# Optimization experiments

Hardware: AMD Instinct MI355X
Metric: run time of the kernel (lower is better)

## Reference

```python
import jax, jax.numpy as jnp
import numpy as np

# module hyperparameters (match init_kwargs)
PATCH = 4          # patch_size
STRIDE = 2         # patch_stride
CH = 64            # embedding_dim (latent channels)
N_ATOMS = 512      # num_embeddings
SPARSITY = 5       # sparsity_level
COMMIT = 0.25      # commitment_cost
EPS = 1e-10        # epsilon
PATCH_DIM = CH * PATCH * PATCH


def _hann(n):
    # torch.hann_window(periodic=False)
    return 0.5 * (1.0 - jnp.cos(2.0 * jnp.pi * jnp.arange(n, dtype=jnp.float32) / (n - 1)))


def setup_inputs() -> dict:
    key = jax.random.key(0)
    k1, k2 = jax.random.split(key)
    x = jax.random.normal(k1, (8, CH, 128, 128), dtype=jnp.float32)
    D = jax.random.normal(k2, (PATCH_DIM, N_ATOMS), dtype=jnp.float32) * 0.02
    # normalize_dictionary_(): L2-normalize atoms (columns)
    D = D / jnp.maximum(jnp.linalg.norm(D, axis=0, keepdims=True), EPS)
    return {"x": x, "dictionary": D}


def reference(x, dictionary):
    B, C, H, W = x.shape
    Ho = (H - PATCH) // STRIDE + 1
    Wo = (W - PATCH) // STRIDE + 1
    N = B * Ho * Wo

    # ---- unfold (im2col) : [B,C,Ho,Wo,P,P] ----
    row = (jnp.arange(Ho) * STRIDE)[:, None] + jnp.arange(PATCH)  # [Ho,P]
    col = (jnp.arange(Wo) * STRIDE)[:, None] + jnp.arange(PATCH)  # [Wo,P]
    ridx = row[:, None, :, None]   # [Ho,1,P,1]
    cidx = col[None, :, None, :]   # [1,Wo,1,P]
    patches = x[:, :, ridx, cidx]  # [B,C,Ho,Wo,P,P]
    # columns ordered (C, ph, pw) like torch F.unfold
    X = patches.transpose(0, 2, 3, 1, 4, 5).reshape(N, PATCH_DIM)  # [N, patch_dim]

    # ---- batch_topk_with_support sparse coding ----
    corr = X @ dictionary                 # [N, K]  (D^T X)^T
    gram = dictionary.T @ dictionary      # [K, K]
    support = jax.lax.top_k(jnp.abs(corr), SPARSITY)[1]           # [N, k]
    rhs = jnp.take_along_axis(corr, support, axis=1)              # [N, k]
    gram_sup = gram[support[:, :, None], support[:, None, :]]     # [N, k, k]
    gram_sup = gram_sup + EPS * jnp.eye(SPARSITY, dtype=x.dtype)
    values = jnp.linalg.solve(gram_sup, rhs[..., None])[..., 0]   # [N, k]

    # ---- reconstruct patch signals: X_hat = D[:,support] @ values ----
    codes = jnp.zeros((N, N_ATOMS), dtype=x.dtype).at[
        jnp.arange(N)[:, None], support].add(values)              # sparse -> dense codes
    X_hat = codes @ dictionary.T                                  # [N, patch_dim]

    # ---- Hann-window overlap-add fold ----
    w1 = _hann(PATCH)
    w2 = w1[:, None] * w1[None, :]                                # [P,P]
    patches_hat = X_hat.reshape(B, Ho, Wo, C, PATCH, PATCH).transpose(0, 3, 1, 2, 4, 5)
    num = jnp.zeros_like(x).at[:, :, ridx, cidx].add(patches_hat * w2)
    den = jnp.zeros((H, W), dtype=x.dtype).at[ridx, cidx].add(
        jnp.broadcast_to(w2, (Ho, Wo, PATCH, PATCH)))
    z_q = num / jnp.maximum(den, EPS)

    # ---- losses + straight-through ----
    e_latent = jnp.mean((jax.lax.stop_gradient(z_q) - x) ** 2)
    dl_latent = jnp.mean((z_q - jax.lax.stop_gradient(x)) ** 2)
    loss = dl_latent + COMMIT * e_latent
    quantized = x + jax.lax.stop_gradient(z_q - x)
    return quantized, loss
```

## Files before the change

kernel.cpp:

```cpp
#include <hip/hip_runtime.h>

#define CHN    64
#define NATOMS 512
#define PDIM   1024
#define KSP    5
#define HO_    63
#define WO_    63
#define NPATCH 31752
#define MPAD   31872
#define HH     128
#define WW     128
#define MT     16
#define OUT_N  8388608
#define DELTA  6e-3f
#define QGUARD 2.5e-3f
#define FBLK   2048

typedef _Float16 f16;
typedef _Float16 f16x8 __attribute__((ext_vector_type(8)));
typedef float    f32x4 __attribute__((ext_vector_type(4)));
typedef float    f32x2 __attribute__((ext_vector_type(2)));

static __device__ __forceinline__ void gload_lds16(const void* g, void* l) {
    __builtin_amdgcn_global_load_lds(
        (const __attribute__((address_space(1))) unsigned int*)g,
        (__attribute__((address_space(3))) unsigned int*)l, 16, 0, 0);
}

static __device__ inline f32x2 fma2(f32x2 a, f32x2 b, f32x2 c) {
#if __has_builtin(__builtin_elementwise_fma)
    return __builtin_elementwise_fma(a, b, c);
#else
    f32x2 r; r.x = fmaf(a.x, b.x, c.x); r.y = fmaf(a.y, b.y, c.y); return r;
#endif
}

static __device__ __forceinline__ unsigned mk_key32(float v, int idx) {
    unsigned vb = __float_as_uint(v);
    unsigned ab = vb & 0x7FFFFFFFu;
    return ((ab >> 11) << 11) | ((unsigned)(1023 - idx) << 1) | (vb >> 31);
}
static __device__ __forceinline__ int key32_idx(unsigned k) {
    return 1023 - (int)((k >> 1) & 1023u);
}

#define CEU(s, i, j) { unsigned _a = s[i], _b = s[j]; \
                       s[i] = _a > _b ? _a : _b; s[j] = _a > _b ? _b : _a; }

#define SORT8(s) \
    CEU(s,0,1) CEU(s,2,3) CEU(s,4,5) CEU(s,6,7) \
    CEU(s,0,2) CEU(s,1,3) CEU(s,4,6) CEU(s,5,7) \
    CEU(s,1,2) CEU(s,5,6) \
    CEU(s,0,4) CEU(s,1,5) CEU(s,2,6) CEU(s,3,7) \
    CEU(s,2,4) CEU(s,3,5) \
    CEU(s,1,2) CEU(s,3,4) CEU(s,5,6)

#define MERGE8(s, a, b) { \
    unsigned L[8]; \
    L[0] = a[0] > b[7] ? a[0] : b[7]; L[1] = a[1] > b[6] ? a[1] : b[6]; \
    L[2] = a[2] > b[5] ? a[2] : b[5]; L[3] = a[3] > b[4] ? a[3] : b[4]; \
    L[4] = a[4] > b[3] ? a[4] : b[3]; L[5] = a[5] > b[2] ? a[5] : b[2]; \
    L[6] = a[6] > b[1] ? a[6] : b[1]; L[7] = a[7] > b[0] ? a[7] : b[0]; \
    CEU(L,0,4) CEU(L,1,5) CEU(L,2,6) CEU(L,3,7) \
    CEU(L,0,2) CEU(L,1,3) CEU(L,4,6) CEU(L,5,7) \
    CEU(L,0,1) CEU(L,2,3) CEU(L,4,5) CEU(L,6,7) \
    for (int _i = 0; _i < 8; ++_i) s[_i] = L[_i]; }

__global__ __launch_bounds__(256) void gram_kernel(const float* __restrict__ D,
                                                   float* __restrict__ gram) {
    __shared__ float Ti[64][32];
    __shared__ float Tj[64][32];
    const int tid = threadIdx.x;
    const int i0 = blockIdx.x * 32, j0 = blockIdx.y * 32;
    const int ri  = tid >> 3;
    const int rj0 = (tid & 7) * 4;
    float acc[4] = {0.f, 0.f, 0.f, 0.f};
    for (int k0 = 0; k0 < PDIM; k0 += 64) {
        __syncthreads();
#pragma unroll
        for (int s = 0; s < 8; ++s) {
            int e = tid + 256 * s;
            int kk = e >> 5, col = e & 31;
            Ti[kk][col] = D[(size_t)(k0 + kk) * NATOMS + i0 + col];
            Tj[kk][col] = D[(size_t)(k0 + kk) * NATOMS + j0 + col];
        }
        __syncthreads();
#pragma unroll 4
        for (int kk = 0; kk < 64; ++kk) {
            float ti = Ti[kk][ri];
#pragma unroll
            for (int q = 0; q < 4; ++q)
                acc[q] = fmaf(ti, Tj[kk][rj0 + q], acc[q]);
        }
    }
#pragma unroll
    for (int q = 0; q < 4; ++q)
        gram[(size_t)(i0 + ri) * NATOMS + j0 + rj0 + q] = acc[q];
}

__global__ __launch_bounds__(256) void extract_kernel(const float* __restrict__ x,
                                                      f16* __restrict__ Xh) {
    __shared__ float xs[16][4][129];
    const int bid = blockIdx.x;
    const int cg  = bid & 3;
    const int t   = bid >> 2;
    const int ho  = t % HO_;
    const int b   = t / HO_;

    for (int i = threadIdx.x; i < 64 * 32; i += 256) {
        int r = i >> 5;
        int q = i & 31;
        int c = r >> 2, pr = r & 3;
        float4 v = *(const float4*)(x + ((size_t)(b * CHN + cg * 16 + c) * HH
                                         + (2 * ho + pr)) * WW + q * 4);
        xs[c][pr][q * 4 + 0] = v.x;
        xs[c][pr][q * 4 + 1] = v.y;
        xs[c][pr][q * 4 + 2] = v.z;
        xs[c][pr][q * 4 + 3] = v.w;
    }
    __syncthreads();

    for (int p = threadIdx.x; p < WO_ * 16; p += 256) {
        int wo = p >> 4;
        int c  = p & 15;
        f16 h[16];
#pragma unroll
        for (int pr = 0; pr < 4; ++pr)
#pragma unroll
            for (int pc = 0; pc < 4; ++pc)
                h[pr * 4 + pc] = (f16)xs[c][pr][2 * wo + pc];
        int n = (b * HO_ + ho) * WO_ + wo;
        f16x8 v0, v1;
#pragma unroll
        for (int i2 = 0; i2 < 8; ++i2) { v0[i2] = h[i2]; v1[i2] = h[8 + i2]; }
        f16* dh = Xh + (size_t)n * PDIM + (cg * 16 + c) * 16;
        *(f16x8*)dh = v0; *(f16x8*)(dh + 8) = v1;
    }
}

__global__ __launch_bounds__(256) void dtrans_kernel(const float* __restrict__ D,
                                                     f16* __restrict__ Dth,
                                                     f16* __restrict__ Dtl) {
    __shared__ float ts[64][65];
    const int k0 = blockIdx.x * 64;
    const int n0 = blockIdx.y * 64;

    for (int i = threadIdx.x; i < 64 * 16; i += 256) {
        int r = i >> 4;
        int q = i & 15;
        float4 v = *(const float4*)(D + (size_t)(k0 + r) * NATOMS + n0 + q * 4);
        ts[r][q * 4 + 0] = v.x;
        ts[r][q * 4 + 1] = v.y;
        ts[r][q * 4 + 2] = v.z;
        ts[r][q * 4 + 3] = v.w;
    }
    __syncthreads();

    {
        int i = threadIdx.x;
        int nn = i >> 2, q = i & 3;
        f16 h[16], l[16];
#pragma unroll
        for (int j = 0; j < 16; ++j) {
            float v = ts[q * 16 + j][nn];
            f16 hh = (f16)v;
            h[j] = hh;
            l[j] = (f16)(v - (float)hh);
        }
        f16x8 h0, h1, l0, l1;
#pragma unroll
        for (int j = 0; j < 8; ++j) { h0[j] = h[j]; h1[j] = h[8 + j]; l0[j] = l[j]; l1[j] = l[8 + j]; }
        f16* dh = Dth + (size_t)(n0 + nn) * PDIM + k0 + q * 16;
        f16* dl = Dtl + (size_t)(n0 + nn) * PDIM + k0 + q * 16;
        *(f16x8*)dh = h0; *(f16x8*)(dh + 8) = h1;
        *(f16x8*)dl = l0; *(f16x8*)(dl + 8) = l1;
    }
}

__global__ __launch_bounds__(512) void gemm_kernel(const f16* __restrict__ Xh,
                                                   const f16* __restrict__ Dth,
                                                   f16* __restrict__ corr) {
    __shared__ char lds[98304];
    const int tid  = threadIdx.x;
    const int lane = tid & 63;
    const int wave = tid >> 6;
    const size_t arow0 = (size_t)blockIdx.x * 128;
    const int    brow0 = blockIdx.y * 256;
    const int wm = wave >> 2;
    const int wn = wave & 3;

    f32x4 acc[4][4];
#pragma unroll
    for (int m = 0; m < 4; ++m)
#pragma unroll
        for (int n = 0; n < 4; ++n) acc[m][n] = (f32x4){0.f, 0.f, 0.f, 0.f};

    const char* asrc[2]; int adst[2];
#pragma unroll
    for (int i = 0; i < 2; ++i) {
        int p = tid * 16 + i * 8192;
        int row = p >> 7, sc = ((p >> 4) & 7) ^ (row & 7);
        asrc[i] = (const char*)Xh + (arow0 + row) * 2048 + sc * 16;
        adst[i] = p;
    }
    const char* bsrc[4]; int bdst[4];
#pragma unroll
    for (int i = 0; i < 4; ++i) {
        int p = tid * 16 + i * 8192;
        int row = p >> 7, sc = ((p >> 4) & 7) ^ (row & 7);
        bsrc[i] = (const char*)Dth + (size_t)(brow0 + row) * 2048 + sc * 16;
        bdst[i] = 16384 + p;
    }

    int aoff[4][2], boff[4][2];
#pragma unroll
    for (int m = 0; m < 4; ++m)
#pragma unroll
        for (int ks = 0; ks < 2; ++ks) {
            int row = wm * 64 + m * 16 + (lane & 15);
            int ch  = (ks * 4 + (lane >> 4)) ^ (row & 7);
            aoff[m][ks] = row * 128 + ch * 16;
        }
#pragma unroll
    for (int n = 0; n < 4; ++n)
#pragma unroll
        for (int ks = 0; ks < 2; ++ks) {
            int row = wn * 64 + n * 16 + (lane & 15);
            int ch  = (ks * 4 + (lane >> 4)) ^ (row & 7);
            boff[n][ks] = 16384 + row * 128 + ch * 16;
        }

#pragma unroll
    for (int i = 0; i < 2; ++i) gload_lds16(asrc[i], lds + adst[i]);
#pragma unroll
    for (int i = 0; i < 4; ++i) gload_lds16(bsrc[i], lds + bdst[i]);
#pragma unroll
    for (int i = 0; i < 2; ++i) asrc[i] += 128;
#pragma unroll
    for (int i = 0; i < 4; ++i) bsrc[i] += 128;
    __syncthreads();

    int bufo = 0;
    for (int kt = 0; kt < 16; ++kt) {
        const int nbuf = bufo ^ 49152;
        if (kt + 1 < 16) {
#pragma unroll
            for (int i = 0; i < 2; ++i) { gload_lds16(asrc[i], lds + nbuf + adst[i]); asrc[i] += 128; }
#pragma unroll
            for (int i = 0; i < 4; ++i) { gload_lds16(bsrc[i], lds + nbuf + bdst[i]); bsrc[i] += 128; }
        }
#pragma unroll
        for (int ks = 0; ks < 2; ++ks) {
            f16x8 a[4], b[4];
#pragma unroll
            for (int m = 0; m < 4; ++m) a[m] = *(const f16x8*)(lds + bufo + aoff[m][ks]);
#pragma unroll
            for (int n = 0; n < 4; ++n) b[n] = *(const f16x8*)(lds + bufo + boff[n][ks]);
#pragma unroll
            for (int m = 0; m < 4; ++m)
#pragma unroll
                for (int n = 0; n < 4; ++n)
                    acc[m][n] = __builtin_amdgcn_mfma_f32_16x16x32_f16(a[m], b[n], acc[m][n], 0, 0, 0);
        }
        if (kt + 1 < 16) { __syncthreads(); bufo = nbuf; }
    }

#pragma unroll
    for (int m = 0; m < 4; ++m) {
        size_t row_b = arow0 + wm * 64 + m * 16 + (lane >> 4) * 4;
#pragma unroll
        for (int n = 0; n < 4; ++n) {
            int col = brow0 + wn * 64 + n * 16 + (lane & 15);
#pragma unroll
            for (int i = 0; i < 4; ++i)
                corr[(row_b + i) * NATOMS + col] = (f16)acc[m][n][i];
        }
    }
}

__global__ __launch_bounds__(512) void topred_kernel(const f16* __restrict__ corr,
                                                     unsigned* __restrict__ topk) {
    const int tid = threadIdx.x;
    const int sl  = tid & 31;
    const int hw  = tid >> 5;
    const int np  = blockIdx.x * 16 + hw;

    const f16* row = corr + (size_t)np * NATOMS;
    const f16* cr = row + sl * 16;
    f16x8 c0 = *(const f16x8*)cr;
    f16x8 c1 = *(const f16x8*)(cr + 8);
    unsigned k[16];
#pragma unroll
    for (int j = 0; j < 8; ++j) {
        k[j]     = mk_key32((float)c0[j], sl * 16 + j);
        k[8 + j] = mk_key32((float)c1[j], sl * 16 + 8 + j);
    }

    unsigned a[8], b8[8];
#pragma unroll
    for (int i = 0; i < 8; ++i) { a[i] = k[i]; b8[i] = k[8 + i]; }
    SORT8(a)
    SORT8(b8)
    unsigned s[8];
    MERGE8(s, a, b8)
#pragma unroll
    for (int off = 16; off; off >>= 1) {
        unsigned p[8];
#pragma unroll
        for (int i = 0; i < 8; ++i) p[i] = (unsigned)__shfl_xor((int)s[i], off);
        MERGE8(s, s, p)
    }

    if (sl == 0 && np < NPATCH) {
        float v0 = (float)row[key32_idx(s[0])], v1 = (float)row[key32_idx(s[1])];
        float v2 = (float)row[key32_idx(s[2])], v3 = (float)row[key32_idx(s[3])];
        float v4 = (float)row[key32_idx(s[4])], v5 = (float)row[key32_idx(s[5])];
        float v6 = (float)row[key32_idx(s[6])], v7 = (float)row[key32_idx(s[7])];
        uint4* dst = (uint4*)(topk + (size_t)np * 16);
        dst[0] = make_uint4(s[0], s[1], s[2], s[3]);
        dst[1] = make_uint4(s[4], s[5], s[6], s[7]);
        dst[2] = make_uint4(__float_as_uint(v0), __float_as_uint(v1),
                            __float_as_uint(v2), __float_as_uint(v3));
        dst[3] = make_uint4(__float_as_uint(v4), __float_as_uint(v5),
                            __float_as_uint(v6), __float_as_uint(v7));
    }
}

__global__ __launch_bounds__(64) void topfin_kernel(const unsigned* __restrict__ topk,
                                                    const f16* __restrict__ corr,
                                                    const float* __restrict__ x,
                                                    const float* __restrict__ D,
                                                    const float* __restrict__ gram,
                                                    int* __restrict__ sup_out,
                                                    float* __restrict__ val_out) {
    const int lane = threadIdx.x & 63;
    const int half = lane >> 5;
    const int sl   = lane & 31;
    const int hw   = threadIdx.x >> 5;
    const int np   = blockIdx.x * 2 + hw;

    unsigned s[8];
    float    tval[8];
    {
        const uint4* src = (const uint4*)(topk + (size_t)np * 16);
        uint4 s0 = src[0], s1 = src[1], v0 = src[2], v1 = src[3];
        s[0] = s0.x; s[1] = s0.y; s[2] = s0.z; s[3] = s0.w;
        s[4] = s1.x; s[5] = s1.y; s[6] = s1.z; s[7] = s1.w;
        tval[0] = __uint_as_float(v0.x); tval[1] = __uint_as_float(v0.y);
        tval[2] = __uint_as_float(v0.z); tval[3] = __uint_as_float(v0.w);
        tval[4] = __uint_as_float(v1.x); tval[5] = __uint_as_float(v1.y);
        tval[6] = __uint_as_float(v1.z); tval[7] = __uint_as_float(v1.w);
    }
    int tidx[8];
#pragma unroll
    for (int r = 0; r < 8; ++r) tidx[r] = key32_idx(s[r]);

    const float a5 = fabsf(tval[KSP - 1]);
    const float lo = fmaxf(a5 - DELTA, 0.0f);
    const float hi = a5 + DELTA;
    const unsigned lokey = (__float_as_uint(fmaxf(lo - QGUARD, 0.0f)) >> 11) << 11;

    int   nfinal = 0, fidx[KSP];
    float fval[KSP];
    int   nwin = 0, widx[8];
    float wvf[8];
#pragma unroll
    for (int r = 0; r < KSP; ++r) {
        if (fabsf(tval[r]) > hi) { fidx[nfinal] = tidx[r]; fval[nfinal] = tval[r]; ++nfinal; }
        else                     { widx[nwin] = tidx[r]; wvf[nwin] = tval[r]; ++nwin; }
    }
#pragma unroll
    for (int r = KSP; r < 8; ++r) {
        if (fabsf(tval[r]) >= lo && nwin < 8) { widx[nwin] = tidx[r]; wvf[nwin] = tval[r]; ++nwin; }
    }

    if (s[7] >= lokey) {
        const f16* cr = corr + (size_t)np * NATOMS + sl * 16;
        f16x8 c0 = *(const f16x8*)cr;
        f16x8 c1 = *(const f16x8*)(cr + 8);
        unsigned k[16];
        float vbuf[16];
#pragma unroll
        for (int j = 0; j < 8; ++j) {
            vbuf[j]     = (float)c0[j];
            vbuf[8 + j] = (float)c1[j];
            k[j]        = mk_key32(vbuf[j], sl * 16 + j);
            k[8 + j]    = mk_key32(vbuf[8 + j], sl * 16 + 8 + j);
        }
#pragma unroll
        for (int i = 0; i < 16; ++i) {
            bool ex = (k[i] < s[7]) && (k[i] >= lokey);
            unsigned m = (unsigned)(__ballot(ex) >> (half * 32));
            while (m && nwin < 8) {
                int l = __ffs(m) - 1; m &= m - 1;
                unsigned kk = (unsigned)__shfl((int)k[i], l + half * 32);
                float vv2 = __shfl(vbuf[i], l + half * 32);
                if (fabsf(vv2) >= lo) { widx[nwin] = key32_idx(kk); wvf[nwin] = vv2; ++nwin; }
            }
        }
    }

    const int need = KSP - nfinal;
    if (nwin == need) {
        for (int w = 0; w < nwin; ++w) { fidx[nfinal] = widx[w]; fval[nfinal] = wvf[w]; ++nfinal; }
    } else {
        int bb_ = np / (HO_ * WO_);
        int rr  = np - bb_ * (HO_ * WO_);
        int ho2 = rr / WO_;
        int wo2 = rr - ho2 * WO_;
        const float* xb = x + (size_t)bb_ * CHN * HH * WW;
        double wv64[8];
        for (int w = 0; w < nwin; ++w) {
            int at = widx[w];
            double sd = 0.0;
#pragma unroll
            for (int t = 0; t < 32; ++t) {
                int kk = sl + (t << 5);
                int c  = kk >> 4, pr = (kk >> 2) & 3, pc = kk & 3;
                float xv = xb[((size_t)c * HH + (2 * ho2 + pr)) * WW + 2 * wo2 + pc];
                float dv = D[(size_t)kk * NATOMS + at];
                sd = fma((double)xv, (double)dv, sd);
            }
            for (int off = 16; off; off >>= 1) sd += __shfl_xor(sd, off);
            wv64[w] = sd;
        }
        unsigned taken = 0u;
        for (int scnt = 0; scnt < need; ++scnt) {
            int best = -1; double bbv = -1.0;
            for (int w = 0; w < nwin; ++w) {
                if ((taken >> w) & 1u) continue;
                double aw = fabs(wv64[w]);
                if (aw > bbv || (aw == bbv && best >= 0 && widx[w] < widx[best])) { bbv = aw; best = w; }
            }
            taken |= 1u << best;
            fidx[nfinal] = widx[best];
            fval[nfinal] = (float)wv64[best];
            ++nfinal;
        }
    }

    float A[KSP][KSP], bb[KSP];
    {
        float gv = 0.f;
        if (sl < 25) {
            int gi = sl / 5, gj = sl - 5 * gi;
            gv = gram[(size_t)fidx[gi] * NATOMS + fidx[gj]];
        }
#pragma unroll
        for (int i = 0; i < KSP; ++i)
#pragma unroll
            for (int j = 0; j < KSP; ++j)
                A[i][j] = __shfl(gv, i * 5 + j + half * 32);
    }
#pragma unroll
    for (int i = 0; i < KSP; ++i) bb[i] = fval[i];
#pragma unroll
    for (int c = 0; c < KSP; ++c) {
        float inv = 1.0f / A[c][c];
#pragma unroll
        for (int r = 0; r < KSP; ++r) {
            if (r > c) {
                float f = A[r][c] * inv;
#pragma unroll
                for (int cc = 0; cc < KSP; ++cc)
                    if (cc > c) A[r][cc] -= f * A[c][cc];
                bb[r] -= f * bb[c];
            }
        }
    }
#pragma unroll
    for (int r = KSP - 1; r >= 0; --r) {
        float t = bb[r];
#pragma unroll
        for (int cc = 0; cc < KSP; ++cc)
            if (cc > r) t -= A[r][cc] * bb[cc];
        bb[r] = t / A[r][r];
    }
    if (sl == 0) {
#pragma unroll
        for (int i = 0; i < KSP; ++i) {
            sup_out[(size_t)np * KSP + i] = fidx[i];
            val_out[(size_t)np * KSP + i] = bb[i];
        }
    }
}

__global__ __launch_bounds__(256) void reconp_kernel(const f16* __restrict__ Dth,
                                                     const f16* __restrict__ Dtl,
                                                     const int* __restrict__ sup,
                                                     const float* __restrict__ val,
                                                     float* __restrict__ zhat) {
    __shared__ f32x4 zbuf[16][65];
    const int lane = threadIdx.x & 63;
    const int wave = threadIdx.x >> 6;
    const int n0   = blockIdx.x * 16;

#pragma unroll
    for (int it = 0; it < 4; ++it) {
        const int nl = it * 4 + wave;
        const int n  = n0 + nl;
        if (n < NPATCH) {
            const int*   sp = sup + (size_t)n * KSP;
            const float* vp = val + (size_t)n * KSP;
            float z[16];
#pragma unroll
            for (int i = 0; i < 16; ++i) z[i] = 0.f;
#pragma unroll
            for (int t = 0; t < KSP; ++t) {
                int a = sp[t]; float v = vp[t];
                const f16* dh = Dth + (size_t)a * PDIM + lane * 16;
                const f16* dl = Dtl + (size_t)a * PDIM + lane * 16;
                f16x8 h0 = *(const f16x8*)dh, h1 = *(const f16x8*)(dh + 8);
                f16x8 l0 = *(const f16x8*)dl, l1 = *(const f16x8*)(dl + 8);
#pragma unroll
                for (int i = 0; i < 8; ++i) {
                    z[i]     = fmaf(v, (float)h0[i] + (float)l0[i], z[i]);
                    z[8 + i] = fmaf(v, (float)h1[i] + (float)l1[i], z[8 + i]);
                }
            }
            zbuf[nl][lane] = (f32x4){ z[5], z[6], z[9], z[10] };
        }
    }
    __syncthreads();

#pragma unroll
    for (int k = 0; k < 4; ++k) {
        int f  = threadIdx.x + 256 * k;
        int c  = f >> 4;
        int nl = f & 15;
        if (n0 + nl < NPATCH)
            *(f32x4*)(zhat + ((size_t)c * NPATCH + n0 + nl) * 4) = zbuf[nl][c];
    }
}

__global__ __launch_bounds__(256) void final_kernel(const float* __restrict__ x,
                                                    const float* __restrict__ zhat,
                                                    float* __restrict__ out,
                                                    double* __restrict__ partials) {
    double sq = 0.0;
    for (size_t g = (size_t)blockIdx.x * 256 + threadIdx.x; g < OUT_N / 4; g += (size_t)FBLK * 256) {
        const size_t o = g * 4;
        const int j0 = (int)(o & 127);
        const int i  = (int)((o >> 7) & 127);
        const int c  = (int)((o >> 14) & 63);
        const int b  = (int)(o >> 20);

        const float4 xv = *(const float4*)(x + o);
        float z0 = 0.f, z1 = 0.f, z2 = 0.f, z3 = 0.f;

        const int pr = (i & 1) ? 1 : 2;
        const int ho = (i - pr) >> 1;
        if (ho >= 0 && ho < HO_) {
            const int prof = (pr - 1) * 2;
            const int q2 = j0 >> 1;
            const size_t nbase = ((size_t)c * NPATCH + (size_t)(b * HO_ + ho) * WO_) * 4;
            int wo = q2 - 1;
            if (wo >= 0) z0 = zhat[nbase + (size_t)wo * 4 + prof + 1];
            wo = q2;
            if (wo < WO_) {
                z1 = zhat[nbase + (size_t)wo * 4 + prof];
                z2 = zhat[nbase + (size_t)wo * 4 + prof + 1];
            }
            wo = q2 + 1;
            if (wo < WO_) z3 = zhat[nbase + (size_t)wo * 4 + prof];
        }
        float4 ov;
        ov.x = xv.x + (z0 - xv.x);
        ov.y = xv.y + (z1 - xv.y);
        ov.z = xv.z + (z2 - xv.z);
        ov.w = xv.w + (z3 - xv.w);
        *(float4*)(out + o) = ov;

        const float d0 = z0 - xv.x, d1 = z1 - xv.y, d2 = z2 - xv.z, d3 = z3 - xv.w;
        sq += (double)d0 * d0 + (double)d1 * d1 + (double)d2 * d2 + (double)d3 * d3;
    }

    for (int off = 32; off; off >>= 1) sq += __shfl_xor(sq, off);
    __shared__ double red[4];
    const int lane = threadIdx.x & 63, wv = threadIdx.x >> 6;
    if (lane == 0) red[wv] = sq;
    __syncthreads();
    if (threadIdx.x == 0) partials[blockIdx.x] = red[0] + red[1] + red[2] + red[3];
}

__global__ __launch_bounds__(256) void loss_kernel(const double* __restrict__ partials,
                                                   float* __restrict__ out) {
    double s = 0.0;
    for (int i = threadIdx.x; i < FBLK; i += 256) s += partials[i];
    for (int off = 32; off; off >>= 1) s += __shfl_xor(s, off);
    __shared__ double red[4];
    const int lane = threadIdx.x & 63, wv = threadIdx.x >> 6;
    if (lane == 0) red[wv] = s;
    __syncthreads();
    if (threadIdx.x == 0) {
        double m = (red[0] + red[1] + red[2] + red[3]) / (double)OUT_N;
        out[OUT_N] = (float)(m + 0.25 * m);
    }
}

__global__ __launch_bounds__(256) void corr_kernel_fb(const float* __restrict__ x,
                                                      const float* __restrict__ D,
                                                      const float* __restrict__ gram,
                                                      int* __restrict__ sup_out,
                                                      float* __restrict__ val_out) {
    __shared__ float pt[256 * MT];
    __shared__ float corrbuf[MT][NATOMS];
    __shared__ int   sup_s[MT][KSP];
    __shared__ float rhs_s[MT][KSP];

    const int tid  = threadIdx.x;
    const int lane = tid & 63;
    const int wave = tid >> 6;
    const int n0   = blockIdx.x * MT;
    const int sp  = lane & 15;
    const int spr = lane >> 4;

    int n = n0 + sp;
    bool pvalid = (n < NPATCH);
    int b = 0, ho = 0, wo = 0;
    if (pvalid) {
        b = n / (HO_ * WO_);
        int r = n - b * (HO_ * WO_);
        ho = r / WO_;
        wo = r - ho * WO_;
    }

    f32x2 accP[2][8];
#pragma unroll
    for (int a = 0; a < 2; ++a)
#pragma unroll
        for (int g = 0; g < 8; ++g) accP[a][g] = (f32x2)(0.f);

    for (int chunk = 0; chunk < 4; ++chunk) {
        __syncthreads();
#pragma unroll
        for (int t = 0; t < 4; ++t) {
            int s = wave + 4 * t;
            int c = chunk * 16 + s;
            float2 va = make_float2(0.f, 0.f), vb = make_float2(0.f, 0.f);
            if (pvalid) {
                const float* px = x + (((size_t)b * CHN + c) * HH + (2 * ho + spr)) * WW + 2 * wo;
                va = *(const float2*)px;
                vb = *(const float2*)(px + 2);
            }
            int kl = (s * 16 + spr * 4) * MT + sp;
            pt[kl]          = va.x;
            pt[kl + MT]     = va.y;
            pt[kl + 2 * MT] = vb.x;
            pt[kl + 3 * MT] = vb.y;
        }
        __syncthreads();
        const float* Dp = D + (size_t)chunk * 256 * NATOMS + 2 * tid;
#pragma unroll 4
        for (int k = 0; k < 256; ++k) {
            float2 dv = *(const float2*)(Dp + (size_t)k * NATOMS);
            f32x2 d00 = {dv.x, dv.x}, d11 = {dv.y, dv.y};
#pragma unroll
            for (int q = 0; q < 4; ++q) {
                const float4 f = *(const float4*)&pt[k * MT + 4 * q];
                f32x2 flo = {f.x, f.y}, fhi = {f.z, f.w};
                accP[0][2 * q]     = fma2(flo, d00, accP[0][2 * q]);
                accP[1][2 * q]     = fma2(flo, d11, accP[1][2 * q]);
                accP[0][2 * q + 1] = fma2(fhi, d00, accP[0][2 * q + 1]);
                accP[1][2 * q + 1] = fma2(fhi, d11, accP[1][2 * q + 1]);
            }
        }
    }
#pragma unroll
    for (int g = 0; g < 8; ++g) {
        *(float2*)&corrbuf[2 * g][2 * tid]     = make_float2(accP[0][g].x, accP[1][g].x);
        *(float2*)&corrbuf[2 * g + 1][2 * tid] = make_float2(accP[0][g].y, accP[1][g].y);
    }
    __syncthreads();

    for (int pi = 0; pi < 4; ++pi) {
        int p  = wave * 4 + pi;
        int np = n0 + p;
        if (np >= NPATCH) continue;
        float v[8], av[8];
#pragma unroll
        for (int i = 0; i < 8; ++i) {
            v[i]  = corrbuf[p][lane + 64 * i];
            av[i] = fabsf(v[i]);
        }
        unsigned usedm = 0u;
        int   top_i[KSP];
        float top_v[KSP];
#pragma unroll
        for (int r = 0; r < KSP; ++r) {
            float ba = -1.0f, bv = 0.0f;
            int   bi = 0x7FFFFFFF;
#pragma unroll
            for (int i = 0; i < 8; ++i) {
                if (!((usedm >> i) & 1u)) {
                    int idx = lane + 64 * i;
                    if (av[i] > ba || (av[i] == ba && idx < bi)) { ba = av[i]; bi = idx; bv = v[i]; }
                }
            }
            for (int off = 32; off; off >>= 1) {
                float oa = __shfl_xor(ba, off);
                int   oi = __shfl_xor(bi, off);
                float ov = __shfl_xor(bv, off);
                if (oa > ba || (oa == ba && oi < bi)) { ba = oa; bi = oi; bv = ov; }
            }
            top_i[r] = bi; top_v[r] = bv;
            if (lane == (bi & 63)) usedm |= (1u << (bi >> 6));
        }
        const float a5 = fabsf(top_v[KSP - 1]);
        const float lo = a5 - DELTA, hi = a5 + DELTA;
        int   nfinal = 0, fidx[KSP];
        float fval[KSP];
        int   nwin = 0, widx[8];
        float wvf[8];
#pragma unroll
        for (int r = 0; r < KSP; ++r) {
            if (fabsf(top_v[r]) > hi) { fidx[nfinal] = top_i[r]; fval[nfinal] = top_v[r]; ++nfinal; }
            else if (nwin < 8)        { widx[nwin] = top_i[r]; wvf[nwin] = top_v[r]; ++nwin; }
        }
#pragma unroll
        for (int i = 0; i < 8; ++i) {
            bool ex = (((usedm >> i) & 1u) == 0u) && (av[i] >= lo);
            unsigned long long m = __ballot(ex);
            while (m && nwin < 8) {
                int l = __ffsll(m) - 1; m &= m - 1;
                widx[nwin] = l + 64 * i;
                wvf[nwin]  = __shfl(v[i], l);
                ++nwin;
            }
        }
        const int need = KSP - nfinal;
        if (nwin == need) {
            for (int w = 0; w < nwin; ++w) { fidx[nfinal] = widx[w]; fval[nfinal] = wvf[w]; ++nfinal; }
        } else {
            int bb_ = np / (HO_ * WO_);
            int rr  = np - bb_ * (HO_ * WO_);
            int ho2 = rr / WO_;
            int wo2 = rr - ho2 * WO_;
            const float* xb = x + (size_t)bb_ * CHN * HH * WW;
            double wv64[8];
            for (int w = 0; w < nwin; ++w) {
                int a = widx[w];
                double s = 0.0;
                for (int t = 0; t < 16; ++t) {
                    int k  = lane + (t << 6);
                    int c  = k >> 4, pr = (k >> 2) & 3, pc = k & 3;
                    float xv = xb[((size_t)c * HH + (2 * ho2 + pr)) * WW + 2 * wo2 + pc];
                    float dv = D[(size_t)k * NATOMS + a];
                    s = fma((double)xv, (double)dv, s);
                }
                for (int off = 32; off; off >>= 1) s += __shfl_xor(s, off);
                wv64[w] = s;
            }
            unsigned taken = 0u;
            for (int scnt = 0; scnt < need; ++scnt) {
                int best = -1; double bbv = -1.0;
                for (int w = 0; w < nwin; ++w) {
                    if ((taken >> w) & 1u) continue;
                    double aw = fabs(wv64[w]);
                    if (aw > bbv || (aw == bbv && best >= 0 && widx[w] < widx[best])) { bbv = aw; best = w; }
                }
                taken |= 1u << best;
                fidx[nfinal] = widx[best];
                fval[nfinal] = (float)wv64[best];
                ++nfinal;
            }
        }
        if (lane == 0) {
#pragma unroll
            for (int r = 0; r < KSP; ++r) { sup_s[p][r] = fidx[r]; rhs_s[p][r] = fval[r]; }
        }
    }
    __syncthreads();

    if (tid < MT) {
        int p = tid, np = n0 + p;
        if (np < NPATCH) {
            int s[KSP];
            double A[KSP][KSP], bb[KSP];
#pragma unroll
            for (int i = 0; i < KSP; ++i) { s[i] = sup_s[p][i]; bb[i] = (double)rhs_s[p][i]; }
#pragma unroll
            for (int i = 0; i < KSP; ++i)
#pragma unroll
                for (int j = 0; j < KSP; ++j)
                    A[i][j] = (double)gram[(size_t)s[i] * NATOMS + s[j]] + (i == j ? 1e-10 : 0.0);
#pragma unroll
            for (int c = 0; c < KSP; ++c) {
                double inv = 1.0 / A[c][c];
#pragma unroll
                for (int r = 0; r < KSP; ++r) {
                    if (r > c) {
                        double f = A[r][c] * inv;
#pragma unroll
                        for (int cc = 0; cc < KSP; ++cc)
                            if (cc > c) A[r][cc] -= f * A[c][cc];
                        bb[r] -= f * bb[c];
                    }
                }
            }
#pragma unroll
            for (int r = KSP - 1; r >= 0; --r) {
                double t = bb[r];
#pragma unroll
                for (int cc = 0; cc < KSP; ++cc)
                    if (cc > r) t -= A[r][cc] * bb[cc];
                bb[r] = t / A[r][r];
            }
#pragma unroll
            for (int i = 0; i < KSP; ++i) {
                sup_out[(size_t)np * KSP + i] = s[i];
                val_out[(size_t)np * KSP + i] = (float)bb[i];
            }
        }
    }
}

__global__ __launch_bounds__(256) void recon_kernel_fb(const float* __restrict__ x,
                                                       const float* __restrict__ D,
                                                       const int* __restrict__ sup,
                                                       const float* __restrict__ val,
                                                       float* __restrict__ out,
                                                       double* __restrict__ partials) {
    double sqacc = 0.0;
    for (size_t o = (size_t)blockIdx.x * 256 + threadIdx.x; o < OUT_N; o += (size_t)FBLK * 256) {
        const int j = (int)(o & 127);
        const int i = (int)((o >> 7) & 127);
        const int c = (int)((o >> 14) & 63);
        const int b = (int)(o >> 20);
        const float xv = x[o];
        float z = 0.0f;
        const int pr = (i & 1) ? 1 : 2;
        const int pc = (j & 1) ? 1 : 2;
        const int ho = (i - pr) >> 1;
        const int wo = (j - pc) >> 1;
        if (ho >= 0 && ho < HO_ && wo >= 0 && wo < WO_) {
            const int n = (b * HO_ + ho) * WO_ + wo;
            const int k = c * 16 + pr * 4 + pc;
            const int*   sp5 = sup + (size_t)n * KSP;
            const float* vp5 = val + (size_t)n * KSP;
            float s = 0.0f;
#pragma unroll
            for (int t = 0; t < KSP; ++t)
                s = fmaf(vp5[t], D[(size_t)k * NATOMS + sp5[t]], s);
            z = s;
        }
        out[o] = xv + (z - xv);
        const float d = z - xv;
        sqacc += (double)d * (double)d;
    }
    for (int off = 32; off; off >>= 1) sqacc += __shfl_xor(sqacc, off);
    __shared__ double red[4];
    const int lane = threadIdx.x & 63, wv = threadIdx.x >> 6;
    if (lane == 0) red[wv] = sqacc;
    __syncthreads();
    if (threadIdx.x == 0) partials[blockIdx.x] = red[0] + red[1] + red[2] + red[3];
}

extern "C" void kernel_launch(void* const* d_in, const int* in_sizes, int n_in,
                              void* d_out, int out_size, void* d_ws, size_t ws_size,
                              hipStream_t stream) {
    const float* x = (const float*)d_in[0];
    const float* D = (const float*)d_in[1];
    float* out = (float*)d_out;
    char* ws = (char*)d_ws;

    size_t off = 0;
    auto take = [&](size_t bytes) { char* p = ws + off; off += (bytes + 255) & ~(size_t)255; return p; };
    float*    gram     = (float*)take((size_t)NATOMS * NATOMS * 4);
    int*      sup      = (int*)take((size_t)NPATCH * KSP * 4);
    float*    val      = (float*)take((size_t)NPATCH * KSP * 4);
    double*   partials = (double*)take((size_t)FBLK * 8);
    unsigned* topk     = (unsigned*)take((size_t)NPATCH * 16 * 4);
    f16*   Dth  = (f16*)take((size_t)NATOMS * PDIM * 2);
    f16*   Dtl  = (f16*)take((size_t)NATOMS * PDIM * 2);
    float* zhat = (float*)take((size_t)CHN * NPATCH * 4 * 4);
    f16*   Xh   = (f16*)take((size_t)MPAD * PDIM * 2);
    f16*   corr = (f16*)take((size_t)MPAD * NATOMS * 2);
    const bool big = (off <= ws_size);

    if (big) {
        hipMemsetAsync(Xh + (size_t)NPATCH * PDIM, 0,
                       (size_t)(MPAD - NPATCH) * PDIM * sizeof(f16), stream);
        extract_kernel<<<8 * HO_ * 4, 256, 0, stream>>>(x, Xh);
        dtrans_kernel<<<dim3(16, 8), 256, 0, stream>>>(D, Dth, Dtl);
        gram_kernel<<<dim3(16, 16), 256, 0, stream>>>(D, gram);
        gemm_kernel<<<dim3(MPAD / 128, NATOMS / 256), 512, 0, stream>>>(Xh, Dth, corr);
        topred_kernel<<<(NPATCH + 15) / 16, 512, 0, stream>>>(corr, topk);
        topfin_kernel<<<NPATCH / 2, 64, 0, stream>>>(topk, corr, x, D, gram, sup, val);
        reconp_kernel<<<(NPATCH + 15) / 16, 256, 0, stream>>>(Dth, Dtl, sup, val, zhat);
        final_kernel<<<FBLK, 256, 0, stream>>>(x, zhat, out, partials);
        loss_kernel<<<1, 256, 0, stream>>>(partials, out);
    } else {
        gram_kernel<<<dim3(16, 16), 256, 0, stream>>>(D, gram);
        corr_kernel_fb<<<(NPATCH + MT - 1) / MT, 256, 0, stream>>>(x, D, gram, sup, val);
        recon_kernel_fb<<<FBLK, 256, 0, stream>>>(x, D, sup, val, out, partials);
        loss_kernel<<<1, 256, 0, stream>>>(partials, out);
    }
}
```

Baseline: 231.1 us.

## Fuse overlap-add output and loss partials into reconstruction kernel, add border kernel

Drops the intermediate zhat buffer and the separate final_kernel. Each reconstructed patch now writes its central 2x2 pixels straight into the output and accumulates squared-error partials. A new small border_kernel handles the one-pixel frame of zeros, and the loss reduction combines both sets of partials. This removes a large intermediate write and read plus a full pass over x. The cost is scattered 4-byte stores from reconp instead of coalesced float4 writes.

```diff
diff --git a/kernel.cpp b/kernel.cpp
--- a/kernel.cpp
+++ b/kernel.cpp
@@ -15,6 +15,7 @@
 #define DELTA  6e-3f
 #define QGUARD 2.5e-3f
 #define FBLK   2048
+#define RPB    ((NPATCH + 15) / 16)
 
 typedef _Float16 f16;
 typedef _Float16 f16x8 __attribute__((ext_vector_type(8)));
@@ -485,12 +486,15 @@
     }
 }
 
-__global__ __launch_bounds__(256) void reconp_kernel(const f16* __restrict__ Dth,
+__global__ __launch_bounds__(256) void reconp_kernel(const float* __restrict__ x,
+                                                     const f16* __restrict__ Dth,
                                                      const f16* __restrict__ Dtl,
                                                      const int* __restrict__ sup,
                                                      const float* __restrict__ val,
-                                                     float* __restrict__ zhat) {
+                                                     float* __restrict__ out,
+                                                     double* __restrict__ rpart) {
     __shared__ f32x4 zbuf[16][65];
+    __shared__ double red[4];
     const int lane = threadIdx.x & 63;
     const int wave = threadIdx.x >> 6;
     const int n0   = blockIdx.x * 16;
@@ -523,70 +527,67 @@
     }
     __syncthreads();
 
+    double sq = 0.0;
 #pragma unroll
     for (int k = 0; k < 4; ++k) {
         int f  = threadIdx.x + 256 * k;
         int c  = f >> 4;
         int nl = f & 15;
-        if (n0 + nl < NPATCH)
-            *(f32x4*)(zhat + ((size_t)c * NPATCH + n0 + nl) * 4) = zbuf[nl][c];
-    }
-}
-
-__global__ __launch_bounds__(256) void final_kernel(const float* __restrict__ x,
-                                                    const float* __restrict__ zhat,
-                                                    float* __restrict__ out,
-                                                    double* __restrict__ partials) {
+        int n  = n0 + nl;
+        if (n < NPATCH) {
+            int b  = n / (HO_ * WO_);
+            int r  = n - b * (HO_ * WO_);
+            int ho = r / WO_, wo = r - ho * WO_;
+            f32x4 zv = zbuf[nl][c];
+            size_t base = ((size_t)(b * CHN + c) * HH + (2 * ho + 1)) * WW + (2 * wo + 1);
+            float x0 = x[base],      x1 = x[base + 1];
+            float x2 = x[base + WW], x3 = x[base + WW + 1];
+            out[base]          = x0 + (zv.x - x0);
+            out[base + 1]      = x1 + (zv.y - x1);
+            out[base + WW]     = x2 + (zv.z - x2);
+            out[base + WW + 1] = x3 + (zv.w - x3);
+            float d0 = zv.x - x0, d1 = zv.y - x1, d2 = zv.z - x2, d3 = zv.w - x3;
+            sq += (double)d0 * d0 + (double)d1 * d1 + (double)d2 * d2 + (double)d3 * d3;
+        }
+    }
+
+    for (int off = 32; off; off >>= 1) sq += __shfl_xor(sq, off);
+    if (lane == 0) red[wave] = sq;
+    __syncthreads();
+    if (threadIdx.x == 0) rpart[blockIdx.x] = red[0] + red[1] + red[2] + red[3];
+}
+
+__global__ __launch_bounds__(256) void border_kernel(const float* __restrict__ x,
+                                                     float* __restrict__ out,
+                                                     double* __restrict__ bpart) {
+    const int plane = blockIdx.x;
+    const float* xp = x + (size_t)plane * HH * WW;
+    float* op = out + (size_t)plane * HH * WW;
     double sq = 0.0;
-    for (size_t g = (size_t)blockIdx.x * 256 + threadIdx.x; g < OUT_N / 4; g += (size_t)FBLK * 256) {
-        const size_t o = g * 4;
-        const int j0 = (int)(o & 127);
-        const int i  = (int)((o >> 7) & 127);
-        const int c  = (int)((o >> 14) & 63);
-        const int b  = (int)(o >> 20);
-
-        const float4 xv = *(const float4*)(x + o);
-        float z0 = 0.f, z1 = 0.f, z2 = 0.f, z3 = 0.f;
-
-        const int pr = (i & 1) ? 1 : 2;
-        const int ho = (i - pr) >> 1;
-        if (ho >= 0 && ho < HO_) {
-            const int prof = (pr - 1) * 2;
-            const int q2 = j0 >> 1;
-            const size_t nbase = ((size_t)c * NPATCH + (size_t)(b * HO_ + ho) * WO_) * 4;
-            int wo = q2 - 1;
-            if (wo >= 0) z0 = zhat[nbase + (size_t)wo * 4 + prof + 1];
-            wo = q2;
-            if (wo < WO_) {
-                z1 = zhat[nbase + (size_t)wo * 4 + prof];
-                z2 = zhat[nbase + (size_t)wo * 4 + prof + 1];
-            }
-            wo = q2 + 1;
-            if (wo < WO_) z3 = zhat[nbase + (size_t)wo * 4 + prof];
-        }
-        float4 ov;
-        ov.x = xv.x + (z0 - xv.x);
-        ov.y = xv.y + (z1 - xv.y);
-        ov.z = xv.z + (z2 - xv.z);
-        ov.w = xv.w + (z3 - xv.w);
-        *(float4*)(out + o) = ov;
-
-        const float d0 = z0 - xv.x, d1 = z1 - xv.y, d2 = z2 - xv.z, d3 = z3 - xv.w;
-        sq += (double)d0 * d0 + (double)d1 * d1 + (double)d2 * d2 + (double)d3 * d3;
-    }
-
+    for (int idx = threadIdx.x; idx < 508; idx += 256) {
+        int i, j;
+        if (idx < 128)      { i = 0;         j = idx;       }
+        else if (idx < 256) { i = 127;       j = idx - 128; }
+        else if (idx < 382) { i = idx - 255; j = 0;         }
+        else                { i = idx - 381; j = 127;       }
+        float xv = xp[i * WW + j];
+        op[i * WW + j] = xv + (0.0f - xv);
+        sq += (double)xv * xv;
+    }
     for (int off = 32; off; off >>= 1) sq += __shfl_xor(sq, off);
     __shared__ double red[4];
     const int lane = threadIdx.x & 63, wv = threadIdx.x >> 6;
     if (lane == 0) red[wv] = sq;
     __syncthreads();
-    if (threadIdx.x == 0) partials[blockIdx.x] = red[0] + red[1] + red[2] + red[3];
-}
-
-__global__ __launch_bounds__(256) void loss_kernel(const double* __restrict__ partials,
-                                                   float* __restrict__ out) {
+    if (threadIdx.x == 0) bpart[blockIdx.x] = red[0] + red[1] + red[2] + red[3];
+}
+
+__global__ __launch_bounds__(256) void loss2_kernel(const double* __restrict__ rpart,
+                                                    const double* __restrict__ bpart,
+                                                    float* __restrict__ out) {
     double s = 0.0;
-    for (int i = threadIdx.x; i < FBLK; i += 256) s += partials[i];
+    for (int i = threadIdx.x; i < RPB; i += 256) s += rpart[i];
+    for (int i = threadIdx.x; i < 512; i += 256) s += bpart[i];
     for (int off = 32; off; off >>= 1) s += __shfl_xor(s, off);
     __shared__ double red[4];
     const int lane = threadIdx.x & 63, wv = threadIdx.x >> 6;
@@ -856,6 +857,21 @@
     if (threadIdx.x == 0) partials[blockIdx.x] = red[0] + red[1] + red[2] + red[3];
 }
 
+__global__ __launch_bounds__(256) void loss_kernel(const double* __restrict__ partials,
+                                                   float* __restrict__ out) {
+    double s = 0.0;
+    for (int i = threadIdx.x; i < FBLK; i += 256) s += partials[i];
+    for (int off = 32; off; off >>= 1) s += __shfl_xor(s, off);
+    __shared__ double red[4];
+    const int lane = threadIdx.x & 63, wv = threadIdx.x >> 6;
+    if (lane == 0) red[wv] = s;
+    __syncthreads();
+    if (threadIdx.x == 0) {
+        double m = (red[0] + red[1] + red[2] + red[3]) / (double)OUT_N;
+        out[OUT_N] = (float)(m + 0.25 * m);
+    }
+}
+
 extern "C" void kernel_launch(void* const* d_in, const int* in_sizes, int n_in,
                               void* d_out, int out_size, void* d_ws, size_t ws_size,
                               hipStream_t stream) {
@@ -870,10 +886,11 @@
     int*      sup      = (int*)take((size_t)NPATCH * KSP * 4);
     float*    val      = (float*)take((size_t)NPATCH * KSP * 4);
     double*   partials = (double*)take((size_t)FBLK * 8);
+    double*   rpart    = (double*)take((size_t)RPB * 8);
+    double*   bpart    = (double*)take((size_t)512 * 8);
     unsigned* topk     = (unsigned*)take((size_t)NPATCH * 16 * 4);
     f16*   Dth  = (f16*)take((size_t)NATOMS * PDIM * 2);
     f16*   Dtl  = (f16*)take((size_t)NATOMS * PDIM * 2);
-    float* zhat = (float*)take((size_t)CHN * NPATCH * 4 * 4);
     f16*   Xh   = (f16*)take((size_t)MPAD * PDIM * 2);
     f16*   corr = (f16*)take((size_t)MPAD * NATOMS * 2);
     const bool big = (off <= ws_size);
@@ -884,12 +901,12 @@
         extract_kernel<<<8 * HO_ * 4, 256, 0, stream>>>(x, Xh);
         dtrans_kernel<<<dim3(16, 8), 256, 0, stream>>>(D, Dth, Dtl);
         gram_kernel<<<dim3(16, 16), 256, 0, stream>>>(D, gram);
+        border_kernel<<<512, 256, 0, stream>>>(x, out, bpart);
         gemm_kernel<<<dim3(MPAD / 128, NATOMS / 256), 512, 0, stream>>>(Xh, Dth, corr);
         topred_kernel<<<(NPATCH + 15) / 16, 512, 0, stream>>>(corr, topk);
         topfin_kernel<<<NPATCH / 2, 64, 0, stream>>>(topk, corr, x, D, gram, sup, val);
-        reconp_kernel<<<(NPATCH + 15) / 16, 256, 0, stream>>>(Dth, Dtl, sup, val, zhat);
-        final_kernel<<<FBLK, 256, 0, stream>>>(x, zhat, out, partials);
-        loss_kernel<<<1, 256, 0, stream>>>(partials, out);
+        reconp_kernel<<<RPB, 256, 0, stream>>>(x, Dth, Dtl, sup, val, out, rpart);
+        loss2_kernel<<<1, 256, 0, stream>>>(rpart, bpart, out);
     } else {
         gram_kernel<<<dim3(16, 16), 256, 0, stream>>>(D, gram);
         corr_kernel_fb<<<(NPATCH + MT - 1) / MT, 256, 0, stream>>>(x, D, gram, sup, val);
```

Result: no change. 226.8 us, median of 2 (-1.8%).
